# Performance work log

Measured on AMD Instinct MI355X. Metric: run time of the kernel, lower is better.

Reference implementation:

```python
import jax, jax.numpy as jnp
import numpy as np

GROUP_SIZE = 32


def dequantize_int4(weight, scales_and_zeros, group_size=GROUP_SIZE):
    """weight: [N, K] int codes in [0,16); scales_and_zeros: [K//gs, N, 2].
    tinygemm convention: w = (q - 8) * scale + zero, groups along K."""
    N, K = weight.shape
    G = K // group_size
    q = weight.astype(scales_and_zeros.dtype).reshape(N, G, group_size)
    scales = scales_and_zeros[:, :, 0].T[:, :, None]  # [N, G, 1]
    zeros = scales_and_zeros[:, :, 1].T[:, :, None]   # [N, G, 1]
    w = (q - 8.0) * scales + zeros
    return w.reshape(N, K)


def setup_inputs() -> dict:
    key = jax.random.key(0)
    k1, k2, k3, k4 = jax.random.split(key, 4)
    M, K, N = 8192, 4096, 12288
    inp = {}
    inp["input"] = jax.random.normal(k1, (M, K), dtype=jnp.float32)
    inp["weight"] = jax.random.randint(k2, (N, K), 0, 16, dtype=jnp.int32)
    # scales small/positive, zeros zero-centered (column 0 = scale, column 1 = zero)
    scales = jax.random.uniform(k3, (K // GROUP_SIZE, N), dtype=jnp.float32) * 0.02 + 1e-3
    zeros = jax.random.normal(k4, (K // GROUP_SIZE, N), dtype=jnp.float32) * 0.05
    inp["scales_and_zeros"] = jnp.stack([scales, zeros], axis=-1)
    inp["bias"] = jax.random.normal(jax.random.fold_in(key, 5), (N,), dtype=jnp.float32)
    return inp


def reference(input, weight, scales_and_zeros, bias):
    # Faithful math of INT4Linear.forward: the tinygemm ops perform a GEMM of
    # input [M,K] against the dequantized int4 weight [N,K] (groupwise
    # scale/zero along K), then add bias. Layout conversions are identity math.
    w_dq = dequantize_int4(weight, scales_and_zeros)  # [N, K]
    y = jnp.einsum("mk,nk->mn", input, w_dq)          # [M, N]
    return y + bias
```

## Files before the change

kernel.cpp:

```cpp
#include <hip/hip_runtime.h>
#include <hip/hip_bf16.h>
#include <cstdint>
#include <cstddef>

#define MM 8192
#define KK 4096
#define NN 12288

typedef __bf16 bf16x8 __attribute__((ext_vector_type(8)));
typedef float  f32x4  __attribute__((ext_vector_type(4)));

__device__ __forceinline__ unsigned short f2bf(float f) {
    union { float f; unsigned int u; } v; v.f = f;
    unsigned int r = v.u + 0x7fffu + ((v.u >> 16) & 1u);
    return (unsigned short)(r >> 16);
}

__device__ __forceinline__ void gload_lds16(const void* g, void* l) {
    __builtin_amdgcn_global_load_lds(
        (__attribute__((address_space(1))) void*)g,
        (__attribute__((address_space(3))) void*)l,
        16, 0, 0);
}

#define FENCE() asm volatile("" ::: "memory")
#define LGKM0() asm volatile("s_waitcnt lgkmcnt(0)" ::: "memory")
#define BARF()  do { FENCE(); __builtin_amdgcn_s_barrier(); FENCE(); } while (0)

__global__ __launch_bounds__(256) void cvt_a_kernel(
    const float* __restrict__ in, unsigned short* __restrict__ out)
{
    size_t i = (size_t)blockIdx.x * 256 + threadIdx.x;
    const float4* p = (const float4*)in;
    float4 x = p[2 * i], y = p[2 * i + 1];
    union { unsigned short h[8]; uint4 v; } u;
    u.h[0] = f2bf(x.x); u.h[1] = f2bf(x.y); u.h[2] = f2bf(x.z); u.h[3] = f2bf(x.w);
    u.h[4] = f2bf(y.x); u.h[5] = f2bf(y.y); u.h[6] = f2bf(y.z); u.h[7] = f2bf(y.w);
    ((uint4*)out)[i] = u.v;
}

__global__ __launch_bounds__(256) void dq_w_kernel(
    const int* __restrict__ w, const float* __restrict__ snz,
    unsigned short* __restrict__ out)
{
    size_t t = (size_t)blockIdx.x * 256 + threadIdx.x;
    int kc = (int)(t & (KK / 8 - 1));
    int n  = (int)(t >> 9);
    int g  = kc >> 2;
    float2 sz = ((const float2*)snz)[(size_t)g * NN + n];
    const int4* wp = (const int4*)w;
    int4 q0 = wp[2 * t], q1 = wp[2 * t + 1];
    union { unsigned short h[8]; uint4 v; } u;
    u.h[0] = f2bf((float)(q0.x - 8) * sz.x + sz.y);
    u.h[1] = f2bf((float)(q0.y - 8) * sz.x + sz.y);
    u.h[2] = f2bf((float)(q0.z - 8) * sz.x + sz.y);
    u.h[3] = f2bf((float)(q0.w - 8) * sz.x + sz.y);
    u.h[4] = f2bf((float)(q1.x - 8) * sz.x + sz.y);
    u.h[5] = f2bf((float)(q1.y - 8) * sz.x + sz.y);
    u.h[6] = f2bf((float)(q1.z - 8) * sz.x + sz.y);
    u.h[7] = f2bf((float)(q1.w - 8) * sz.x + sz.y);
    ((uint4*)out)[t] = u.v;
}

#define BM 256
#define BN 256
#define BK 64
#define TT (KK / BK)

__global__ __launch_bounds__(512, 2) void gemm256_kernel(
    const unsigned short* __restrict__ A,
    const unsigned short* __restrict__ Bw,
    const float* __restrict__ bias,
    float* __restrict__ C)
{
    __shared__ char lds[131072];

    const int tid  = threadIdx.x;
    const int lane = tid & 63;
    const int wave = tid >> 6;
    const int wm   = wave >> 2;
    const int wn   = wave & 3;

    const int NTN = NN / BN;
    const int nwg = (MM / BM) * NTN;
    const int cpx = nwg >> 3;
    int wg = ((int)blockIdx.x & 7) * cpx + ((int)blockIdx.x >> 3);
    const int tm = wg / NTN;
    const int tn = wg - tm * NTN;

    f32x4 acc[8][4] = {};

    const int lrow = lane >> 3;
    const int lc   = (lane & 7) ^ lrow;
    const unsigned short* aSrc = A  + (size_t)(tm * BM + wave * 8 + lrow) * KK + lc * 8;
    const unsigned short* bSrc = Bw + (size_t)(tn * BN + wave * 8 + lrow) * KK + lc * 8;
    const int wblk = wave * 1024;

#define STAGE(srcBase, rowsOff, kOff, ldsOff) do {                                     \
        gload_lds16((srcBase) + (size_t)(rowsOff) * KK + (kOff), lds + (ldsOff) + wblk);            \
        gload_lds16((srcBase) + (size_t)((rowsOff) + 64) * KK + (kOff), lds + (ldsOff) + 8192 + wblk); \
    } while (0)

    const int r7  = lane & 7;
    const int l15 = lane & 15;
    const int c0  = (((lane >> 4)    ) ^ r7) * 16;
    const int c1  = (((lane >> 4) + 4) ^ r7) * 16;
    const int aoff = (wm * 128 + l15) * 128;
    const int boff = (wn * 64  + l15) * 128;

    STAGE(aSrc, 0,   0, 0);
    STAGE(aSrc, 128, 0, 16384);
    STAGE(bSrc, 0,   0, 32768);
    STAGE(bSrc, 128, 0, 32768 + 16384);
    if (TT > 1) {
        STAGE(aSrc, 0,   BK, 65536);
        STAGE(aSrc, 128, BK, 65536 + 16384);
    }
    asm volatile("s_waitcnt vmcnt(4)" ::: "memory");
    BARF();

#pragma unroll 2
    for (int t = 0; t < TT; ++t) {
        const int cb = t & 1, nb = cb ^ 1;
        const char* Ab = lds + cb * 65536;
        const char* Bb = lds + cb * 65536 + 32768;

        bf16x8 a0[8];
#pragma unroll
        for (int mf = 0; mf < 8; ++mf)
            a0[mf] = *(const bf16x8*)(Ab + aoff + mf * 2048 + c0);
        bf16x8 p0b0 = *(const bf16x8*)(Bb + boff + 0 * 2048 + c0);
        bf16x8 p0b1 = *(const bf16x8*)(Bb + boff + 1 * 2048 + c0);
        if (t + 1 < TT) STAGE(bSrc, 0, (t + 1) * BK, nb * 65536 + 32768);
        BARF(); LGKM0();
        __builtin_amdgcn_s_setprio(1);
#pragma unroll
        for (int mf = 0; mf < 8; ++mf) {
            acc[mf][0] = __builtin_amdgcn_mfma_f32_16x16x32_bf16(a0[mf], p0b0, acc[mf][0], 0, 0, 0);
            acc[mf][1] = __builtin_amdgcn_mfma_f32_16x16x32_bf16(a0[mf], p0b1, acc[mf][1], 0, 0, 0);
        }
        __builtin_amdgcn_s_setprio(0);
        BARF();

        bf16x8 a1[8];
#pragma unroll
        for (int mf = 0; mf < 8; ++mf)
            a1[mf] = *(const bf16x8*)(Ab + aoff + mf * 2048 + c1);
        bf16x8 p1b2 = *(const bf16x8*)(Bb + boff + 2 * 2048 + c0);
        bf16x8 p1b3 = *(const bf16x8*)(Bb + boff + 3 * 2048 + c0);
        if (t + 1 < TT) STAGE(bSrc, 128, (t + 1) * BK, nb * 65536 + 32768 + 16384);
        BARF(); LGKM0();
        __builtin_amdgcn_s_setprio(1);
#pragma unroll
        for (int mf = 0; mf < 8; ++mf) {
            acc[mf][2] = __builtin_amdgcn_mfma_f32_16x16x32_bf16(a0[mf], p1b2, acc[mf][2], 0, 0, 0);
            acc[mf][3] = __builtin_amdgcn_mfma_f32_16x16x32_bf16(a0[mf], p1b3, acc[mf][3], 0, 0, 0);
        }
        __builtin_amdgcn_s_setprio(0);
        BARF();

        bf16x8 p2b0 = *(const bf16x8*)(Bb + boff + 0 * 2048 + c1);
        bf16x8 p2b1 = *(const bf16x8*)(Bb + boff + 1 * 2048 + c1);
        if (t + 2 < TT) STAGE(aSrc, 0, (t + 2) * BK, cb * 65536);
        BARF(); LGKM0();
        __builtin_amdgcn_s_setprio(1);
#pragma unroll
        for (int mf = 0; mf < 8; ++mf) {
            acc[mf][0] = __builtin_amdgcn_mfma_f32_16x16x32_bf16(a1[mf], p2b0, acc[mf][0], 0, 0, 0);
            acc[mf][1] = __builtin_amdgcn_mfma_f32_16x16x32_bf16(a1[mf], p2b1, acc[mf][1], 0, 0, 0);
        }
        __builtin_amdgcn_s_setprio(0);
        BARF();

        bf16x8 p3b2 = *(const bf16x8*)(Bb + boff + 2 * 2048 + c1);
        bf16x8 p3b3 = *(const bf16x8*)(Bb + boff + 3 * 2048 + c1);
        if (t + 2 < TT) STAGE(aSrc, 128, (t + 2) * BK, cb * 65536 + 16384);
        BARF(); LGKM0();
        __builtin_amdgcn_s_setprio(1);
#pragma unroll
        for (int mf = 0; mf < 8; ++mf) {
            acc[mf][2] = __builtin_amdgcn_mfma_f32_16x16x32_bf16(a1[mf], p3b2, acc[mf][2], 0, 0, 0);
            acc[mf][3] = __builtin_amdgcn_mfma_f32_16x16x32_bf16(a1[mf], p3b3, acc[mf][3], 0, 0, 0);
        }
        __builtin_amdgcn_s_setprio(0);
        if (t < TT - 1) {
            if (t + 2 < TT) { asm volatile("s_waitcnt vmcnt(4)" ::: "memory"); }
            else            { asm volatile("s_waitcnt vmcnt(0)" ::: "memory"); }
            BARF();
        }
    }
#undef STAGE

    const int crow = tm * BM + wm * 128 + (lane >> 4) * 4;
    const int ccol = tn * BN + wn * 64 + l15;
    float bv[4];
#pragma unroll
    for (int nf = 0; nf < 4; ++nf) bv[nf] = bias[ccol + nf * 16];
#pragma unroll
    for (int mf = 0; mf < 8; ++mf)
#pragma unroll
        for (int nf = 0; nf < 4; ++nf)
#pragma unroll
            for (int j = 0; j < 4; ++j)
                C[(size_t)(crow + mf * 16 + j) * NN + ccol + nf * 16] =
                    acc[mf][nf][j] + bv[nf];
}

__global__ __launch_bounds__(256) void gemm_fused_kernel(
    const float* __restrict__ Af,
    const int* __restrict__ Wq,
    const float* __restrict__ snz,
    const float* __restrict__ bias,
    float* __restrict__ C)
{
    __shared__ alignas(16) unsigned short As[128 * 64];
    __shared__ alignas(16) unsigned short Bs[128 * 64];

    const int tid  = threadIdx.x;
    const int lane = tid & 63;
    const int wave = tid >> 6;

    const int NTN = NN / 128;
    const int nwg = (MM / 128) * NTN;
    const int cpx = nwg >> 3;
    int wg = ((int)blockIdx.x & 7) * cpx + ((int)blockIdx.x >> 3);
    const int tm = wg / NTN;
    const int tn = wg - tm * NTN;

    const int wm = wave >> 1, wn = wave & 1;

    f32x4 acc[4][4] = {};

    const int r7  = lane & 7;
    const int pc0 = (((lane >> 4)    ) ^ r7) * 16;
    const int pc1 = (((lane >> 4) + 4) ^ r7) * 16;
    const int arow = wm * 64 + (lane & 15);
    const int brow = wn * 64 + (lane & 15);
    const char* AsR = (const char*)As;
    const char* BsR = (const char*)Bs;

    const int frow = tid >> 1;
    const int fh   = tid & 1;
    const int frx  = frow & 7;

    for (int k0 = 0; k0 < KK; k0 += 64) {
        {
            const float* ap = Af + (size_t)(tm * 128 + frow) * KK + k0 + fh * 32;
#pragma unroll
            for (int c = 0; c < 4; ++c) {
                float4 x = ((const float4*)ap)[2 * c];
                float4 y = ((const float4*)ap)[2 * c + 1];
                union { unsigned short h[8]; uint4 v; } u;
                u.h[0] = f2bf(x.x); u.h[1] = f2bf(x.y); u.h[2] = f2bf(x.z); u.h[3] = f2bf(x.w);
                u.h[4] = f2bf(y.x); u.h[5] = f2bf(y.y); u.h[6] = f2bf(y.z); u.h[7] = f2bf(y.w);
                int lc2 = fh * 4 + c;
                *(uint4*)&As[frow * 64 + ((lc2 ^ frx) * 8)] = u.v;
            }
        }
        {
            const int nrow = tn * 128 + frow;
            const int* wp = Wq + (size_t)nrow * KK + k0 + fh * 32;
            float2 sz = ((const float2*)snz)[(size_t)((k0 >> 5) + fh) * NN + nrow];
#pragma unroll
            for (int c = 0; c < 4; ++c) {
                int4 q0 = ((const int4*)wp)[2 * c];
                int4 q1 = ((const int4*)wp)[2 * c + 1];
                union { unsigned short h[8]; uint4 v; } u;
                u.h[0] = f2bf((float)(q0.x - 8) * sz.x + sz.y);
                u.h[1] = f2bf((float)(q0.y - 8) * sz.x + sz.y);
                u.h[2] = f2bf((float)(q0.z - 8) * sz.x + sz.y);
                u.h[3] = f2bf((float)(q0.w - 8) * sz.x + sz.y);
                u.h[4] = f2bf((float)(q1.x - 8) * sz.x + sz.y);
                u.h[5] = f2bf((float)(q1.y - 8) * sz.x + sz.y);
                u.h[6] = f2bf((float)(q1.z - 8) * sz.x + sz.y);
                u.h[7] = f2bf((float)(q1.w - 8) * sz.x + sz.y);
                int lc2 = fh * 4 + c;
                *(uint4*)&Bs[frow * 64 + ((lc2 ^ frx) * 8)] = u.v;
            }
        }
        __syncthreads();
        {
            bf16x8 af[4], bfr[4];
#pragma unroll
            for (int x = 0; x < 4; ++x) {
                af[x]  = *(const bf16x8*)(AsR + (arow + x * 16) * 128 + pc0);
                bfr[x] = *(const bf16x8*)(BsR + (brow + x * 16) * 128 + pc0);
            }
#pragma unroll
            for (int mi = 0; mi < 4; ++mi)
#pragma unroll
                for (int ni = 0; ni < 4; ++ni)
                    acc[mi][ni] = __builtin_amdgcn_mfma_f32_16x16x32_bf16(
                        af[mi], bfr[ni], acc[mi][ni], 0, 0, 0);
        }
        {
            bf16x8 af[4], bfr[4];
#pragma unroll
            for (int x = 0; x < 4; ++x) {
                af[x]  = *(const bf16x8*)(AsR + (arow + x * 16) * 128 + pc1);
                bfr[x] = *(const bf16x8*)(BsR + (brow + x * 16) * 128 + pc1);
            }
#pragma unroll
            for (int mi = 0; mi < 4; ++mi)
#pragma unroll
                for (int ni = 0; ni < 4; ++ni)
                    acc[mi][ni] = __builtin_amdgcn_mfma_f32_16x16x32_bf16(
                        af[mi], bfr[ni], acc[mi][ni], 0, 0, 0);
        }
        __syncthreads();
    }

    const int crow = tm * 128 + wm * 64 + (lane >> 4) * 4;
    const int ccol = tn * 128 + wn * 64 + (lane & 15);
    float bv[4];
#pragma unroll
    for (int ni = 0; ni < 4; ++ni) bv[ni] = bias[ccol + ni * 16];
#pragma unroll
    for (int mi = 0; mi < 4; ++mi)
#pragma unroll
        for (int ni = 0; ni < 4; ++ni)
#pragma unroll
            for (int j = 0; j < 4; ++j)
                C[(size_t)(crow + mi * 16 + j) * NN + ccol + ni * 16] =
                    acc[mi][ni][j] + bv[ni];
}

extern "C" void kernel_launch(void* const* d_in, const int* in_sizes, int n_in,
                              void* d_out, int out_size, void* d_ws, size_t ws_size,
                              hipStream_t stream)
{
    const float* inA  = (const float*)d_in[0];
    const int*   Wq   = (const int*)d_in[1];
    const float* snz  = (const float*)d_in[2];
    const float* bias = (const float*)d_in[3];
    float* out = (float*)d_out;

    const size_t needA = (size_t)MM * KK * 2;
    const size_t needW = (size_t)NN * KK * 2;

    if (ws_size >= needA + needW) {
        unsigned short* Abf = (unsigned short*)d_ws;
        unsigned short* Wbf = (unsigned short*)((char*)d_ws + needA);
        cvt_a_kernel<<<(MM * KK / 8) / 256, 256, 0, stream>>>(inA, Abf);
        dq_w_kernel<<<(NN * KK / 8) / 256, 256, 0, stream>>>(Wq, snz, Wbf);
        gemm256_kernel<<<(MM / BM) * (NN / BN), 512, 0, stream>>>(Abf, Wbf, bias, out);
    } else {
        gemm_fused_kernel<<<(MM / 128) * (NN / 128), 256, 0, stream>>>(
            inA, Wq, snz, bias, out);
    }
}
```

Baseline: 818.8 us.

## Triple-buffer B tiles in LDS to prefetch two K-steps ahead

Enlarges LDS to 160 KB and gives the B operand a three-slot ring buffer, so both A and B tiles are prefetched two K-iterations ahead instead of B only one. The wait before each iteration now allows eight outstanding loads. The aim is to hide more global-load latency behind the MFMA work. The cost is that 160 KB of LDS per block likely drops occupancy from the requested two blocks per CU to one, and the loop loses its unroll-by-2 hint and adds modulo-3 index arithmetic.

New measurement: 817.7 us. About the same (-0.1%).

```diff
diff --git a/kernel.cpp b/kernel.cpp
--- a/kernel.cpp
+++ b/kernel.cpp
@@ -73,7 +73,7 @@
     const float* __restrict__ bias,
     float* __restrict__ C)
 {
-    __shared__ char lds[131072];
+    __shared__ char lds[163840];
 
     const int tid  = threadIdx.x;
     const int lane = tid & 63;
@@ -96,9 +96,9 @@
     const unsigned short* bSrc = Bw + (size_t)(tn * BN + wave * 8 + lrow) * KK + lc * 8;
     const int wblk = wave * 1024;
 
-#define STAGE(srcBase, rowsOff, kOff, ldsOff) do {                                     \
-        gload_lds16((srcBase) + (size_t)(rowsOff) * KK + (kOff), lds + (ldsOff) + wblk);            \
-        gload_lds16((srcBase) + (size_t)((rowsOff) + 64) * KK + (kOff), lds + (ldsOff) + 8192 + wblk); \
+#define STAGE(srcBase, rowsOff, kOff, ldsPtr) do {                                          \
+        gload_lds16((srcBase) + (size_t)(rowsOff) * KK + (kOff), (ldsPtr) + wblk);          \
+        gload_lds16((srcBase) + (size_t)((rowsOff) + 64) * KK + (kOff), (ldsPtr) + 8192 + wblk); \
     } while (0)
 
     const int r7  = lane & 7;
@@ -108,22 +108,26 @@
     const int aoff = (wm * 128 + l15) * 128;
     const int boff = (wn * 64  + l15) * 128;
 
-    STAGE(aSrc, 0,   0, 0);
-    STAGE(aSrc, 128, 0, 16384);
-    STAGE(bSrc, 0,   0, 32768);
-    STAGE(bSrc, 128, 0, 32768 + 16384);
-    if (TT > 1) {
-        STAGE(aSrc, 0,   BK, 65536);
-        STAGE(aSrc, 128, BK, 65536 + 16384);
-    }
-    asm volatile("s_waitcnt vmcnt(4)" ::: "memory");
+    STAGE(aSrc, 0,   0, lds + 0);
+    STAGE(aSrc, 128, 0, lds + 16384);
+    STAGE(bSrc, 0,   0, lds + 65536);
+    STAGE(bSrc, 128, 0, lds + 65536 + 16384);
+    STAGE(aSrc, 0,   BK, lds + 32768);
+    STAGE(aSrc, 128, BK, lds + 32768 + 16384);
+    STAGE(bSrc, 0,   BK, lds + 65536 + 32768);
+    STAGE(bSrc, 128, BK, lds + 65536 + 32768 + 16384);
+    asm volatile("s_waitcnt vmcnt(8)" ::: "memory");
     BARF();
 
-#pragma unroll 2
+    int bRead = 0;
     for (int t = 0; t < TT; ++t) {
-        const int cb = t & 1, nb = cb ^ 1;
-        const char* Ab = lds + cb * 65536;
-        const char* Bb = lds + cb * 65536 + 32768;
+        const char* Ab = lds + ((t & 1) << 15);
+        const char* Bb = lds + 65536 + (bRead << 15);
+        int bs = bRead + 2; if (bs >= 3) bs -= 3;
+        char* Bst = lds + 65536 + (bs << 15);
+        char* Ast = lds + ((t & 1) << 15);
+        const bool pf = (t + 2 < TT);
+        const int kpf = (t + 2) * BK;
 
         bf16x8 a0[8];
 #pragma unroll
@@ -131,7 +135,7 @@
             a0[mf] = *(const bf16x8*)(Ab + aoff + mf * 2048 + c0);
         bf16x8 p0b0 = *(const bf16x8*)(Bb + boff + 0 * 2048 + c0);
         bf16x8 p0b1 = *(const bf16x8*)(Bb + boff + 1 * 2048 + c0);
-        if (t + 1 < TT) STAGE(bSrc, 0, (t + 1) * BK, nb * 65536 + 32768);
+        if (pf) STAGE(bSrc, 0, kpf, Bst);
         BARF(); LGKM0();
         __builtin_amdgcn_s_setprio(1);
 #pragma unroll
@@ -148,7 +152,7 @@
             a1[mf] = *(const bf16x8*)(Ab + aoff + mf * 2048 + c1);
         bf16x8 p1b2 = *(const bf16x8*)(Bb + boff + 2 * 2048 + c0);
         bf16x8 p1b3 = *(const bf16x8*)(Bb + boff + 3 * 2048 + c0);
-        if (t + 1 < TT) STAGE(bSrc, 128, (t + 1) * BK, nb * 65536 + 32768 + 16384);
+        if (pf) STAGE(bSrc, 128, kpf, Bst + 16384);
         BARF(); LGKM0();
         __builtin_amdgcn_s_setprio(1);
 #pragma unroll
@@ -161,7 +165,7 @@
 
         bf16x8 p2b0 = *(const bf16x8*)(Bb + boff + 0 * 2048 + c1);
         bf16x8 p2b1 = *(const bf16x8*)(Bb + boff + 1 * 2048 + c1);
-        if (t + 2 < TT) STAGE(aSrc, 0, (t + 2) * BK, cb * 65536);
+        if (pf) STAGE(aSrc, 0, kpf, Ast);
         BARF(); LGKM0();
         __builtin_amdgcn_s_setprio(1);
 #pragma unroll
@@ -174,7 +178,7 @@
 
         bf16x8 p3b2 = *(const bf16x8*)(Bb + boff + 2 * 2048 + c1);
         bf16x8 p3b3 = *(const bf16x8*)(Bb + boff + 3 * 2048 + c1);
-        if (t + 2 < TT) STAGE(aSrc, 128, (t + 2) * BK, cb * 65536 + 16384);
+        if (pf) STAGE(aSrc, 128, kpf, Ast + 16384);
         BARF(); LGKM0();
         __builtin_amdgcn_s_setprio(1);
 #pragma unroll
@@ -184,10 +188,11 @@
         }
         __builtin_amdgcn_s_setprio(0);
         if (t < TT - 1) {
-            if (t + 2 < TT) { asm volatile("s_waitcnt vmcnt(4)" ::: "memory"); }
-            else            { asm volatile("s_waitcnt vmcnt(0)" ::: "memory"); }
+            if (pf) { asm volatile("s_waitcnt vmcnt(8)" ::: "memory"); }
+            else    { asm volatile("s_waitcnt vmcnt(0)" ::: "memory"); }
             BARF();
         }
+        bRead = bRead + 1; if (bRead >= 3) bRead -= 3;
     }
 #undef STAGE
 
```

## Cut per-iteration barriers in GEMM main loop and regroup LDS reads with prefetch

Applied to the files above, without the earlier changes.

Rewrites the K-loop schedule so each iteration uses one mid-iteration barrier plus the end barrier, down from four barriers and four LDS-wait points. The B prefetch for the next tile is now issued as one batch at the start, and the A prefetch for t+2 as one batch before the last MFMA group. The aim is to cut synchronisation stalls so more MFMA work overlaps the LDS reads. The risk is a race: the A prefetch writes into the current buffer's A region while other waves may still be reading a1 from it. Correctness then depends on the single mid-iteration barrier coming after all A reads, which it does, since the a1 loads and the LGKM0 wait sit before that barrier.

Measured after the change: 813.5 us. Within noise of the previous version (-0.6%).

```diff
diff --git a/kernel.cpp b/kernel.cpp
--- a/kernel.cpp
+++ b/kernel.cpp
@@ -96,9 +96,9 @@
     const unsigned short* bSrc = Bw + (size_t)(tn * BN + wave * 8 + lrow) * KK + lc * 8;
     const int wblk = wave * 1024;
 
-#define STAGE(srcBase, rowsOff, kOff, ldsOff) do {                                     \
-        gload_lds16((srcBase) + (size_t)(rowsOff) * KK + (kOff), lds + (ldsOff) + wblk);            \
-        gload_lds16((srcBase) + (size_t)((rowsOff) + 64) * KK + (kOff), lds + (ldsOff) + 8192 + wblk); \
+#define STAGE(srcBase, rowsOff, kOff, ldsPtr) do {                                          \
+        gload_lds16((srcBase) + (size_t)(rowsOff) * KK + (kOff), (ldsPtr) + wblk);          \
+        gload_lds16((srcBase) + (size_t)((rowsOff) + 64) * KK + (kOff), (ldsPtr) + 8192 + wblk); \
     } while (0)
 
     const int r7  = lane & 7;
@@ -108,87 +108,80 @@
     const int aoff = (wm * 128 + l15) * 128;
     const int boff = (wn * 64  + l15) * 128;
 
-    STAGE(aSrc, 0,   0, 0);
-    STAGE(aSrc, 128, 0, 16384);
-    STAGE(bSrc, 0,   0, 32768);
-    STAGE(bSrc, 128, 0, 32768 + 16384);
-    if (TT > 1) {
-        STAGE(aSrc, 0,   BK, 65536);
-        STAGE(aSrc, 128, BK, 65536 + 16384);
-    }
+    STAGE(aSrc, 0,   0, lds + 0);
+    STAGE(aSrc, 128, 0, lds + 16384);
+    STAGE(bSrc, 0,   0, lds + 32768);
+    STAGE(bSrc, 128, 0, lds + 32768 + 16384);
+    STAGE(aSrc, 0,   BK, lds + 65536);
+    STAGE(aSrc, 128, BK, lds + 65536 + 16384);
     asm volatile("s_waitcnt vmcnt(4)" ::: "memory");
     BARF();
 
+#define MFMA8(AARR, BREG, NF)                                                     \
+    _Pragma("unroll")                                                             \
+    for (int mf = 0; mf < 8; ++mf)                                                \
+        acc[mf][NF] = __builtin_amdgcn_mfma_f32_16x16x32_bf16(                    \
+            AARR[mf], BREG, acc[mf][NF], 0, 0, 0);
+
 #pragma unroll 2
     for (int t = 0; t < TT; ++t) {
-        const int cb = t & 1, nb = cb ^ 1;
-        const char* Ab = lds + cb * 65536;
-        const char* Bb = lds + cb * 65536 + 32768;
-
+        const char* Ab = lds + ((t & 1) << 16);
+        const char* Bb = Ab + 32768;
+        char* BstN = lds + (((t & 1) ^ 1) << 16) + 32768;
+        char* AstN = lds + ((t & 1) << 16);
+        const bool pfB = (t + 1 < TT);
+        const bool pfA = (t + 2 < TT);
+        const int kB = (t + 1) * BK;
+        const int kA = (t + 2) * BK;
+
+        bf16x8 b00 = *(const bf16x8*)(Bb + boff + 0 * 2048 + c0);
+        bf16x8 b01 = *(const bf16x8*)(Bb + boff + 1 * 2048 + c0);
         bf16x8 a0[8];
 #pragma unroll
         for (int mf = 0; mf < 8; ++mf)
             a0[mf] = *(const bf16x8*)(Ab + aoff + mf * 2048 + c0);
-        bf16x8 p0b0 = *(const bf16x8*)(Bb + boff + 0 * 2048 + c0);
-        bf16x8 p0b1 = *(const bf16x8*)(Bb + boff + 1 * 2048 + c0);
-        if (t + 1 < TT) STAGE(bSrc, 0, (t + 1) * BK, nb * 65536 + 32768);
-        BARF(); LGKM0();
+        if (pfB) {
+            STAGE(bSrc, 0,   kB, BstN);
+            STAGE(bSrc, 128, kB, BstN + 16384);
+        }
         __builtin_amdgcn_s_setprio(1);
-#pragma unroll
-        for (int mf = 0; mf < 8; ++mf) {
-            acc[mf][0] = __builtin_amdgcn_mfma_f32_16x16x32_bf16(a0[mf], p0b0, acc[mf][0], 0, 0, 0);
-            acc[mf][1] = __builtin_amdgcn_mfma_f32_16x16x32_bf16(a0[mf], p0b1, acc[mf][1], 0, 0, 0);
-        }
+        MFMA8(a0, b00, 0); MFMA8(a0, b01, 1);
         __builtin_amdgcn_s_setprio(0);
-        BARF();
+
+        bf16x8 b02 = *(const bf16x8*)(Bb + boff + 2 * 2048 + c0);
+        bf16x8 b03 = *(const bf16x8*)(Bb + boff + 3 * 2048 + c0);
+        __builtin_amdgcn_s_setprio(1);
+        MFMA8(a0, b02, 2); MFMA8(a0, b03, 3);
+        __builtin_amdgcn_s_setprio(0);
 
         bf16x8 a1[8];
 #pragma unroll
         for (int mf = 0; mf < 8; ++mf)
             a1[mf] = *(const bf16x8*)(Ab + aoff + mf * 2048 + c1);
-        bf16x8 p1b2 = *(const bf16x8*)(Bb + boff + 2 * 2048 + c0);
-        bf16x8 p1b3 = *(const bf16x8*)(Bb + boff + 3 * 2048 + c0);
-        if (t + 1 < TT) STAGE(bSrc, 128, (t + 1) * BK, nb * 65536 + 32768 + 16384);
-        BARF(); LGKM0();
+        bf16x8 b10 = *(const bf16x8*)(Bb + boff + 0 * 2048 + c1);
+        bf16x8 b11 = *(const bf16x8*)(Bb + boff + 1 * 2048 + c1);
+        LGKM0();
+        BARF();
         __builtin_amdgcn_s_setprio(1);
-#pragma unroll
-        for (int mf = 0; mf < 8; ++mf) {
-            acc[mf][2] = __builtin_amdgcn_mfma_f32_16x16x32_bf16(a0[mf], p1b2, acc[mf][2], 0, 0, 0);
-            acc[mf][3] = __builtin_amdgcn_mfma_f32_16x16x32_bf16(a0[mf], p1b3, acc[mf][3], 0, 0, 0);
-        }
+        MFMA8(a1, b10, 0); MFMA8(a1, b11, 1);
         __builtin_amdgcn_s_setprio(0);
-        BARF();
-
-        bf16x8 p2b0 = *(const bf16x8*)(Bb + boff + 0 * 2048 + c1);
-        bf16x8 p2b1 = *(const bf16x8*)(Bb + boff + 1 * 2048 + c1);
-        if (t + 2 < TT) STAGE(aSrc, 0, (t + 2) * BK, cb * 65536);
-        BARF(); LGKM0();
+
+        bf16x8 b12 = *(const bf16x8*)(Bb + boff + 2 * 2048 + c1);
+        bf16x8 b13 = *(const bf16x8*)(Bb + boff + 3 * 2048 + c1);
+        if (pfA) {
+            STAGE(aSrc, 0,   kA, AstN);
+            STAGE(aSrc, 128, kA, AstN + 16384);
+        }
         __builtin_amdgcn_s_setprio(1);
-#pragma unroll
-        for (int mf = 0; mf < 8; ++mf) {
-            acc[mf][0] = __builtin_amdgcn_mfma_f32_16x16x32_bf16(a1[mf], p2b0, acc[mf][0], 0, 0, 0);
-            acc[mf][1] = __builtin_amdgcn_mfma_f32_16x16x32_bf16(a1[mf], p2b1, acc[mf][1], 0, 0, 0);
-        }
-        __builtin_amdgcn_s_setprio(0);
-        BARF();
-
-        bf16x8 p3b2 = *(const bf16x8*)(Bb + boff + 2 * 2048 + c1);
-        bf16x8 p3b3 = *(const bf16x8*)(Bb + boff + 3 * 2048 + c1);
-        if (t + 2 < TT) STAGE(aSrc, 128, (t + 2) * BK, cb * 65536 + 16384);
-        BARF(); LGKM0();
-        __builtin_amdgcn_s_setprio(1);
-#pragma unroll
-        for (int mf = 0; mf < 8; ++mf) {
-            acc[mf][2] = __builtin_amdgcn_mfma_f32_16x16x32_bf16(a1[mf], p3b2, acc[mf][2], 0, 0, 0);
-            acc[mf][3] = __builtin_amdgcn_mfma_f32_16x16x32_bf16(a1[mf], p3b3, acc[mf][3], 0, 0, 0);
-        }
+        MFMA8(a1, b12, 2); MFMA8(a1, b13, 3);
         __builtin_amdgcn_s_setprio(0);
         if (t < TT - 1) {
-            if (t + 2 < TT) { asm volatile("s_waitcnt vmcnt(4)" ::: "memory"); }
-            else            { asm volatile("s_waitcnt vmcnt(0)" ::: "memory"); }
+            if (pfA) { asm volatile("s_waitcnt vmcnt(4)" ::: "memory"); }
+            else     { asm volatile("s_waitcnt vmcnt(0)" ::: "memory"); }
             BARF();
         }
     }
+#undef MFMA8
 #undef STAGE
 
     const int crow = tm * BM + wm * 128 + (lane >> 4) * 4;
```

## Replace pipelined 256x256 GEMM with single-buffered 256x128 high-occupancy kernel

Applied to the files above, without the earlier changes.

Replaces the double-buffered, finely interleaved 256x256 bf16 MFMA GEMM with a simpler 256x128 tile kernel. The new kernel uses a single 48KB LDS buffer, fewer accumulators per wave and launch bounds allowing four blocks per CU. It relies on thread-level parallelism across blocks instead of software pipelining to hide global-load latency. In exchange it gives up the explicit prefetch overlap, waits on vmcnt(0) every K step, and lowers arithmetic intensity per tile, which raises LDS and global traffic.

Result: slower. 894.1 us (+9.2%).

```diff
diff --git a/kernel.cpp b/kernel.cpp
--- a/kernel.cpp
+++ b/kernel.cpp
@@ -24,7 +24,6 @@
 }
 
 #define FENCE() asm volatile("" ::: "memory")
-#define LGKM0() asm volatile("s_waitcnt lgkmcnt(0)" ::: "memory")
 #define BARF()  do { FENCE(); __builtin_amdgcn_s_barrier(); FENCE(); } while (0)
 
 __global__ __launch_bounds__(256) void cvt_a_kernel(
@@ -63,23 +62,23 @@
 }
 
 #define BM 256
-#define BN 256
+#define BN 128
 #define BK 64
 #define TT (KK / BK)
 
-__global__ __launch_bounds__(512, 2) void gemm256_kernel(
+__global__ __launch_bounds__(512, 4) void gemm_tlp_kernel(
     const unsigned short* __restrict__ A,
     const unsigned short* __restrict__ Bw,
     const float* __restrict__ bias,
     float* __restrict__ C)
 {
-    __shared__ char lds[131072];
+    __shared__ char lds[49152];
 
     const int tid  = threadIdx.x;
     const int lane = tid & 63;
     const int wave = tid >> 6;
-    const int wm   = wave >> 2;
-    const int wn   = wave & 3;
+    const int wr   = wave >> 1;
+    const int wc   = wave & 1;
 
     const int NTN = NN / BN;
     const int nwg = (MM / BM) * NTN;
@@ -88,7 +87,7 @@
     const int tm = wg / NTN;
     const int tn = wg - tm * NTN;
 
-    f32x4 acc[8][4] = {};
+    f32x4 acc[4][4] = {};
 
     const int lrow = lane >> 3;
     const int lc   = (lane & 7) ^ lrow;
@@ -96,114 +95,74 @@
     const unsigned short* bSrc = Bw + (size_t)(tn * BN + wave * 8 + lrow) * KK + lc * 8;
     const int wblk = wave * 1024;
 
-#define STAGE(srcBase, rowsOff, kOff, ldsOff) do {                                     \
-        gload_lds16((srcBase) + (size_t)(rowsOff) * KK + (kOff), lds + (ldsOff) + wblk);            \
-        gload_lds16((srcBase) + (size_t)((rowsOff) + 64) * KK + (kOff), lds + (ldsOff) + 8192 + wblk); \
-    } while (0)
-
     const int r7  = lane & 7;
     const int l15 = lane & 15;
     const int c0  = (((lane >> 4)    ) ^ r7) * 16;
     const int c1  = (((lane >> 4) + 4) ^ r7) * 16;
-    const int aoff = (wm * 128 + l15) * 128;
-    const int boff = (wn * 64  + l15) * 128;
-
-    STAGE(aSrc, 0,   0, 0);
-    STAGE(aSrc, 128, 0, 16384);
-    STAGE(bSrc, 0,   0, 32768);
-    STAGE(bSrc, 128, 0, 32768 + 16384);
-    if (TT > 1) {
-        STAGE(aSrc, 0,   BK, 65536);
-        STAGE(aSrc, 128, BK, 65536 + 16384);
+    const int aoff = (wr * 64 + l15) * 128;
+    const int boff = (wc * 64 + l15) * 128;
+
+#pragma unroll 1
+    for (int t = 0; t < TT; ++t) {
+        const int k0 = t * BK;
+
+#pragma unroll
+        for (int i = 0; i < 4; ++i)
+            gload_lds16(aSrc + (size_t)(i * 64) * KK + k0, lds + i * 8192 + wblk);
+#pragma unroll
+        for (int i = 0; i < 2; ++i)
+            gload_lds16(bSrc + (size_t)(i * 64) * KK + k0, lds + 32768 + i * 8192 + wblk);
+        asm volatile("s_waitcnt vmcnt(0)" ::: "memory");
+        BARF();
+
+        {
+            bf16x8 a_[4], b_[4];
+#pragma unroll
+            for (int x = 0; x < 4; ++x) {
+                a_[x] = *(const bf16x8*)(lds + aoff + x * 2048 + c0);
+                b_[x] = *(const bf16x8*)(lds + 32768 + boff + x * 2048 + c0);
+            }
+            __builtin_amdgcn_s_setprio(1);
+#pragma unroll
+            for (int mi = 0; mi < 4; ++mi)
+#pragma unroll
+                for (int ni = 0; ni < 4; ++ni)
+                    acc[mi][ni] = __builtin_amdgcn_mfma_f32_16x16x32_bf16(
+                        a_[mi], b_[ni], acc[mi][ni], 0, 0, 0);
+            __builtin_amdgcn_s_setprio(0);
+        }
+        {
+            bf16x8 a_[4], b_[4];
+#pragma unroll
+            for (int x = 0; x < 4; ++x) {
+                a_[x] = *(const bf16x8*)(lds + aoff + x * 2048 + c1);
+                b_[x] = *(const bf16x8*)(lds + 32768 + boff + x * 2048 + c1);
+            }
+            __builtin_amdgcn_s_setprio(1);
+#pragma unroll
+            for (int mi = 0; mi < 4; ++mi)
+#pragma unroll
+                for (int ni = 0; ni < 4; ++ni)
+                    acc[mi][ni] = __builtin_amdgcn_mfma_f32_16x16x32_bf16(
+                        a_[mi], b_[ni], acc[mi][ni], 0, 0, 0);
+            __builtin_amdgcn_s_setprio(0);
+        }
+        BARF();
     }
-    asm volatile("s_waitcnt vmcnt(4)" ::: "memory");
-    BARF();
-
-#pragma unroll 2
-    for (int t = 0; t < TT; ++t) {
-        const int cb = t & 1, nb = cb ^ 1;
-        const char* Ab = lds + cb * 65536;
-        const char* Bb = lds + cb * 65536 + 32768;
-
-        bf16x8 a0[8];
-#pragma unroll
-        for (int mf = 0; mf < 8; ++mf)
-            a0[mf] = *(const bf16x8*)(Ab + aoff + mf * 2048 + c0);
-        bf16x8 p0b0 = *(const bf16x8*)(Bb + boff + 0 * 2048 + c0);
-        bf16x8 p0b1 = *(const bf16x8*)(Bb + boff + 1 * 2048 + c0);
-        if (t + 1 < TT) STAGE(bSrc, 0, (t + 1) * BK, nb * 65536 + 32768);
-        BARF(); LGKM0();
-        __builtin_amdgcn_s_setprio(1);
-#pragma unroll
-        for (int mf = 0; mf < 8; ++mf) {
-            acc[mf][0] = __builtin_amdgcn_mfma_f32_16x16x32_bf16(a0[mf], p0b0, acc[mf][0], 0, 0, 0);
-            acc[mf][1] = __builtin_amdgcn_mfma_f32_16x16x32_bf16(a0[mf], p0b1, acc[mf][1], 0, 0, 0);
-        }
-        __builtin_amdgcn_s_setprio(0);
-        BARF();
-
-        bf16x8 a1[8];
-#pragma unroll
-        for (int mf = 0; mf < 8; ++mf)
-            a1[mf] = *(const bf16x8*)(Ab + aoff + mf * 2048 + c1);
-        bf16x8 p1b2 = *(const bf16x8*)(Bb + boff + 2 * 2048 + c0);
-        bf16x8 p1b3 = *(const bf16x8*)(Bb + boff + 3 * 2048 + c0);
-        if (t + 1 < TT) STAGE(bSrc, 128, (t + 1) * BK, nb * 65536 + 32768 + 16384);
-        BARF(); LGKM0();
-        __builtin_amdgcn_s_setprio(1);
-#pragma unroll
-        for (int mf = 0; mf < 8; ++mf) {
-            acc[mf][2] = __builtin_amdgcn_mfma_f32_16x16x32_bf16(a0[mf], p1b2, acc[mf][2], 0, 0, 0);
-            acc[mf][3] = __builtin_amdgcn_mfma_f32_16x16x32_bf16(a0[mf], p1b3, acc[mf][3], 0, 0, 0);
-        }
-        __builtin_amdgcn_s_setprio(0);
-        BARF();
-
-        bf16x8 p2b0 = *(const bf16x8*)(Bb + boff + 0 * 2048 + c1);
-        bf16x8 p2b1 = *(const bf16x8*)(Bb + boff + 1 * 2048 + c1);
-        if (t + 2 < TT) STAGE(aSrc, 0, (t + 2) * BK, cb * 65536);
-        BARF(); LGKM0();
-        __builtin_amdgcn_s_setprio(1);
-#pragma unroll
-        for (int mf = 0; mf < 8; ++mf) {
-            acc[mf][0] = __builtin_amdgcn_mfma_f32_16x16x32_bf16(a1[mf], p2b0, acc[mf][0], 0, 0, 0);
-            acc[mf][1] = __builtin_amdgcn_mfma_f32_16x16x32_bf16(a1[mf], p2b1, acc[mf][1], 0, 0, 0);
-        }
-        __builtin_amdgcn_s_setprio(0);
-        BARF();
-
-        bf16x8 p3b2 = *(const bf16x8*)(Bb + boff + 2 * 2048 + c1);
-        bf16x8 p3b3 = *(const bf16x8*)(Bb + boff + 3 * 2048 + c1);
-        if (t + 2 < TT) STAGE(aSrc, 128, (t + 2) * BK, cb * 65536 + 16384);
-        BARF(); LGKM0();
-        __builtin_amdgcn_s_setprio(1);
-#pragma unroll
-        for (int mf = 0; mf < 8; ++mf) {
-            acc[mf][2] = __builtin_amdgcn_mfma_f32_16x16x32_bf16(a1[mf], p3b2, acc[mf][2], 0, 0, 0);
-            acc[mf][3] = __builtin_amdgcn_mfma_f32_16x16x32_bf16(a1[mf], p3b3, acc[mf][3], 0, 0, 0);
-        }
-        __builtin_amdgcn_s_setprio(0);
-        if (t < TT - 1) {
-            if (t + 2 < TT) { asm volatile("s_waitcnt vmcnt(4)" ::: "memory"); }
-            else            { asm volatile("s_waitcnt vmcnt(0)" ::: "memory"); }
-            BARF();
-        }
-    }
-#undef STAGE
-
-    const int crow = tm * BM + wm * 128 + (lane >> 4) * 4;
-    const int ccol = tn * BN + wn * 64 + l15;
+
+    const int crow = tm * BM + wr * 64 + (lane >> 4) * 4;
+    const int ccol = tn * BN + wc * 64 + l15;
     float bv[4];
 #pragma unroll
-    for (int nf = 0; nf < 4; ++nf) bv[nf] = bias[ccol + nf * 16];
-#pragma unroll
-    for (int mf = 0; mf < 8; ++mf)
-#pragma unroll
-        for (int nf = 0; nf < 4; ++nf)
+    for (int ni = 0; ni < 4; ++ni) bv[ni] = bias[ccol + ni * 16];
+#pragma unroll
+    for (int mi = 0; mi < 4; ++mi)
+#pragma unroll
+        for (int ni = 0; ni < 4; ++ni)
 #pragma unroll
             for (int j = 0; j < 4; ++j)
-                C[(size_t)(crow + mf * 16 + j) * NN + ccol + nf * 16] =
-                    acc[mf][nf][j] + bv[nf];
+                C[(size_t)(crow + mi * 16 + j) * NN + ccol + ni * 16] =
+                    acc[mi][ni][j] + bv[ni];
 }
 
 __global__ __launch_bounds__(256) void gemm_fused_kernel(
@@ -343,7 +302,7 @@
         unsigned short* Wbf = (unsigned short*)((char*)d_ws + needA);
         cvt_a_kernel<<<(MM * KK / 8) / 256, 256, 0, stream>>>(inA, Abf);
         dq_w_kernel<<<(NN * KK / 8) / 256, 256, 0, stream>>>(Wq, snz, Wbf);
-        gemm256_kernel<<<(MM / BM) * (NN / BN), 512, 0, stream>>>(Abf, Wbf, bias, out);
+        gemm_tlp_kernel<<<(MM / BM) * (NN / BN), 512, 0, stream>>>(Abf, Wbf, bias, out);
     } else {
         gemm_fused_kernel<<<(MM / 128) * (NN / 128), 256, 0, stream>>>(
             inA, Wq, snz, bias, out);
```
